# Performance work log

Hardware: AMD Instinct MI355X
Metric: run time of the kernel (lower is better)

## Reference

```python
import jax, jax.numpy as jnp
import numpy as np

N, L, S, C, H = 8, 1024, 1024, 256, 8
D = C // H  # 32

def setup_inputs() -> dict:
    key = jax.random.key(0)
    ks = jax.random.split(key, 9)
    sc = 1.0 / np.sqrt(C)
    return {
        "x": jax.random.normal(ks[0], (N, L, C), jnp.float32),
        "source1": jax.random.normal(ks[1], (N, S, C), jnp.float32),
        "x_embedding": jax.random.normal(ks[2], (N, L, C), jnp.float32),
        "source_embedding": jax.random.normal(ks[3], (N, S, C), jnp.float32),
        "Wq": jax.random.normal(ks[4], (C, C), jnp.float32) * sc,
        "Wk": jax.random.normal(ks[5], (C, C), jnp.float32) * sc,
        "Wv": jax.random.normal(ks[6], (C, C), jnp.float32) * sc,
        "Wp": jax.random.normal(ks[7], (C, C), jnp.float32) * sc,
        "bp": jnp.zeros((C,), jnp.float32),
    }

def reference(x, source1, x_embedding, source_embedding, Wq, Wk, Wv, Wp, bp):
    bs = x.shape[0]
    # torch `query += x_embedding` is IN-PLACE on x (same for source1),
    # so value projections also see embedding-added inputs.
    xq = x + x_embedding            # [N, L, C]
    sk = source1 + source_embedding  # [N, S, C]
    q = (xq @ Wq.T).reshape(bs, -1, H, D)   # [N, L, H, D]
    k = (sk @ Wk.T).reshape(bs, -1, H, D)   # [N, S, H, D]
    v1 = (xq @ Wv.T).reshape(bs, -1, H, D)  # [N, L, H, D]
    v2 = (sk @ Wv.T).reshape(bs, -1, H, D)  # [N, S, H, D]
    # Bilinear attention: softmax(q.k) aggregates v2, gated elementwise by v1.
    scores = jnp.einsum("nlhd,nshd->nlsh", q, k) / jnp.sqrt(jnp.float32(D))
    attn = jax.nn.softmax(scores, axis=2)          # softmax over source dim S
    message = v1 * jnp.einsum("nlsh,nshd->nlhd", attn, v2)  # [N, L, H, D]
    message = message.reshape(bs, -1, C)           # [N, L, C]
    return message @ Wp.T + bp
```

## Files before the change

kernel.cpp:

```cpp
#include <hip/hip_runtime.h>
#include <hip/hip_bf16.h>


typedef __bf16 bf16_t;
using bf16x8 = __attribute__((ext_vector_type(8))) __bf16;
using f32x4  = __attribute__((ext_vector_type(4))) float;

#define NB 8
#define LL 1024
#define SS 1024
#define CC 256
#define HH 8
#define DD 32
#define MTOK (NB * LL)

#define QSCALE (0.17677669529663688f * 1.4426950408889634f)

static __device__ __forceinline__ f32x4 mfma16(bf16x8 a, bf16x8 b, f32x4 c) {
  return __builtin_amdgcn_mfma_f32_16x16x32_bf16(a, b, c, 0, 0, 0);
}
static __device__ __forceinline__ float fexp2(float x) {
  return __builtin_amdgcn_exp2f(x);
}

__global__ __launch_bounds__(256) void wprep_kernel(
    const float* __restrict__ wq, const float* __restrict__ wk,
    const float* __restrict__ wv, const float* __restrict__ wp,
    bf16_t* __restrict__ Wall) {
  const int i = blockIdx.x * 256 + threadIdx.x;
  const int w = i >> 14, j = i & 16383;
  const float4* src = (const float4*)(w == 0 ? wq : w == 1 ? wk : w == 2 ? wv : wp);
  float4 v = src[j];
  bf16_t t4[4] __attribute__((aligned(8))) = {(bf16_t)v.x, (bf16_t)v.y,
                                              (bf16_t)v.z, (bf16_t)v.w};
  *(uint2*)(Wall + (size_t)w * CC * CC + 4 * (size_t)j) = *(const uint2*)t4;
}

__global__ __launch_bounds__(512) void proj_kernel(
    const float* __restrict__ x, const float* __restrict__ xe,
    const float* __restrict__ s1, const float* __restrict__ se,
    const bf16_t* __restrict__ Wall,
    bf16_t* __restrict__ Qw, bf16_t* __restrict__ Kw,
    bf16_t* __restrict__ V1w, bf16_t* __restrict__ V2T) {
  __shared__ __align__(16) bf16_t a_lds[64][264];

  const int tid = threadIdx.x;
  const int lane = tid & 63;
  const int wid = tid >> 6;
  const int r = lane & 15, g = lane >> 4;
  const int bm = blockIdx.x * 64;
  const int z = blockIdx.y;

  const float* A0 = z ? s1 : x;
  const float* A1 = z ? se : xe;
  const bf16_t* W0 = Wall + (size_t)z * CC * CC;
  const bf16_t* W1 = Wall + 2 * (size_t)CC * CC;

#pragma unroll
  for (int i = 0; i < 8; ++i) {
    const int f = i * 512 + tid;
    const int row = f >> 6, c4 = f & 63;
    float4 va = *(const float4*)(A0 + (size_t)(bm + row) * CC + c4 * 4);
    float4 vb = *(const float4*)(A1 + (size_t)(bm + row) * CC + c4 * 4);
    bf16_t t4[4] __attribute__((aligned(8))) = {
        (bf16_t)(va.x + vb.x), (bf16_t)(va.y + vb.y), (bf16_t)(va.z + vb.z),
        (bf16_t)(va.w + vb.w)};
    *(uint2*)&a_lds[row][c4 * 4] = *(const uint2*)t4;
  }
  __syncthreads();

  const int col_b0 = wid * 32;

  f32x4 acc0[4][2] = {};
  f32x4 acc1[4][2] = {};
#pragma unroll
  for (int k0 = 0; k0 < CC; k0 += 32) {
    bf16x8 a[4];
#pragma unroll
    for (int i = 0; i < 4; ++i)
      a[i] = *(const bf16x8*)&a_lds[i * 16 + r][k0 + g * 8];
    bf16x8 b00 = *(const bf16x8*)(W0 + (size_t)(col_b0 + r) * CC + k0 + g * 8);
    bf16x8 b01 = *(const bf16x8*)(W0 + (size_t)(col_b0 + 16 + r) * CC + k0 + g * 8);
    bf16x8 b10 = *(const bf16x8*)(W1 + (size_t)(col_b0 + r) * CC + k0 + g * 8);
    bf16x8 b11 = *(const bf16x8*)(W1 + (size_t)(col_b0 + 16 + r) * CC + k0 + g * 8);
#pragma unroll
    for (int i = 0; i < 4; ++i) {
      acc0[i][0] = mfma16(a[i], b00, acc0[i][0]);
      acc0[i][1] = mfma16(a[i], b01, acc0[i][1]);
      acc1[i][0] = mfma16(a[i], b10, acc1[i][0]);
      acc1[i][1] = mfma16(a[i], b11, acc1[i][1]);
    }
  }

#pragma unroll
  for (int i = 0; i < 4; ++i) {
#pragma unroll
    for (int j = 0; j < 2; ++j) {
      const int row_base = bm + i * 16 + g * 4;
      const int col = col_b0 + j * 16 + r;
      if (z == 0) {
#pragma unroll
        for (int t = 0; t < 4; ++t) {
          Qw[(size_t)(row_base + t) * CC + col] =
              (bf16_t)(acc0[i][j][t] * QSCALE);
          V1w[(size_t)(row_base + t) * CC + col] = (bf16_t)acc1[i][j][t];
        }
      } else {
#pragma unroll
        for (int t = 0; t < 4; ++t)
          Kw[(size_t)(row_base + t) * CC + col] = (bf16_t)acc0[i][j][t];
        const int n = row_base >> 10;
        const int s = row_base & (SS - 1);
        const int h = col >> 5;
        const int d = col & (DD - 1);
        bf16_t t4[4] __attribute__((aligned(8)));
#pragma unroll
        for (int t = 0; t < 4; ++t) t4[t] = (bf16_t)acc1[i][j][t];
        *(uint2*)(V2T + ((size_t)((n * HH + h) * DD + d)) * SS + s) =
            *(const uint2*)t4;
      }
    }
  }
}

__global__ __launch_bounds__(256) void attn_kernel(
    const bf16_t* __restrict__ Qw, const bf16_t* __restrict__ Kw,
    const bf16_t* __restrict__ V1w, const bf16_t* __restrict__ V2T,
    bf16_t* __restrict__ MSG) {
  __shared__ __align__(16) bf16_t k_lds[2][128][40];
  __shared__ __align__(16) bf16_t v_lds[2][32][136];
  __shared__ __align__(16) bf16_t p_sub[4][32][136];

  const int tid = threadIdx.x;
  const int lane = tid & 63;
  const int wid = tid >> 6;
  const int r = lane & 15, g = lane >> 4;

  const int bid = blockIdx.x;
  const int work = (bid & 7) * 64 + (bid >> 3);
  const int grp = work >> 3;
  const int lt = work & 7;
  const int n = grp >> 3;
  const int h = grp & 7;
  const int l0 = lt * 128;
  const size_t tokQ = (size_t)n * LL + l0 + wid * 32;

  const bf16x8 qf0 = *(const bf16x8*)(Qw + (tokQ + r) * CC + h * DD + g * 8);
  const bf16x8 qf1 = *(const bf16x8*)(Qw + (tokQ + 16 + r) * CC + h * DD + g * 8);
  const bf16_t* Kb = Kw + ((size_t)n * SS) * CC + h * DD;
  const bf16_t* Vt = V2T + ((size_t)(n * HH + h)) * DD * SS;

  const int ktr = tid >> 2, ktq = tid & 3;
  const int vtr = tid >> 3, vtq = tid & 7;

  float lr0 = 0.f, lr1 = 0.f;
  const f32x4 zero = {0.f, 0.f, 0.f, 0.f};
  f32x4 o00 = zero, o01 = zero;
  f32x4 o10 = zero, o11 = zero;

  uint4 kra = *(const uint4*)(Kb + (size_t)ktr * CC + ktq * 8);
  uint4 krb = *(const uint4*)(Kb + (size_t)(64 + ktr) * CC + ktq * 8);
  uint4 vra = *(const uint4*)(Vt + (size_t)vtr * SS + vtq * 8);
  uint4 vrb = *(const uint4*)(Vt + (size_t)vtr * SS + 64 + vtq * 8);
  *(uint4*)&k_lds[0][ktr][ktq * 8] = kra;
  *(uint4*)&k_lds[0][64 + ktr][ktq * 8] = krb;
  *(uint4*)&v_lds[0][vtr][vtq * 8] = vra;
  *(uint4*)&v_lds[0][vtr][64 + vtq * 8] = vrb;
  __syncthreads();

  for (int c = 0; c < 8; ++c) {
    const int cur = c & 1;
    if (c < 7) {
      const int s1 = (c + 1) * 128;
      kra = *(const uint4*)(Kb + (size_t)(s1 + ktr) * CC + ktq * 8);
      krb = *(const uint4*)(Kb + (size_t)(s1 + 64 + ktr) * CC + ktq * 8);
      vra = *(const uint4*)(Vt + (size_t)vtr * SS + s1 + vtq * 8);
      vrb = *(const uint4*)(Vt + (size_t)vtr * SS + s1 + 64 + vtq * 8);
    }

    f32x4 pt0[8], pt1[8];
#pragma unroll
    for (int m = 0; m < 8; ++m) {
      bf16x8 kf = *(const bf16x8*)&k_lds[cur][m * 16 + r][g * 8];
      pt0[m] = mfma16(kf, qf0, zero);
      pt1[m] = mfma16(kf, qf1, zero);
    }

#pragma unroll
    for (int m = 0; m < 8; ++m) {
      float a0 = fexp2(pt0[m][0]), a1 = fexp2(pt0[m][1]);
      float a2 = fexp2(pt0[m][2]), a3 = fexp2(pt0[m][3]);
      float b0 = fexp2(pt1[m][0]), b1 = fexp2(pt1[m][1]);
      float b2 = fexp2(pt1[m][2]), b3 = fexp2(pt1[m][3]);
      lr0 += (a0 + a1) + (a2 + a3);
      lr1 += (b0 + b1) + (b2 + b3);
      bf16_t pa[4] __attribute__((aligned(8))) = {(bf16_t)a0, (bf16_t)a1,
                                                  (bf16_t)a2, (bf16_t)a3};
      bf16_t pb[4] __attribute__((aligned(8))) = {(bf16_t)b0, (bf16_t)b1,
                                                  (bf16_t)b2, (bf16_t)b3};
      *(uint2*)&p_sub[wid][r][m * 16 + g * 4] = *(const uint2*)pa;
      *(uint2*)&p_sub[wid][16 + r][m * 16 + g * 4] = *(const uint2*)pb;
    }

#pragma unroll
    for (int u = 0; u < 4; ++u) {
      bf16x8 pf0 = *(const bf16x8*)&p_sub[wid][r][u * 32 + g * 8];
      bf16x8 pf1 = *(const bf16x8*)&p_sub[wid][16 + r][u * 32 + g * 8];
      bf16x8 va = *(const bf16x8*)&v_lds[cur][r][u * 32 + g * 8];
      bf16x8 vb = *(const bf16x8*)&v_lds[cur][16 + r][u * 32 + g * 8];
      o00 = mfma16(va, pf0, o00);
      o01 = mfma16(vb, pf0, o01);
      o10 = mfma16(va, pf1, o10);
      o11 = mfma16(vb, pf1, o11);
    }

    if (c < 7) {
      *(uint4*)&k_lds[cur ^ 1][ktr][ktq * 8] = kra;
      *(uint4*)&k_lds[cur ^ 1][64 + ktr][ktq * 8] = krb;
      *(uint4*)&v_lds[cur ^ 1][vtr][vtq * 8] = vra;
      *(uint4*)&v_lds[cur ^ 1][vtr][64 + vtq * 8] = vrb;
    }
    __syncthreads();
  }

  lr0 += __shfl_xor(lr0, 16);
  lr0 += __shfl_xor(lr0, 32);
  lr1 += __shfl_xor(lr1, 16);
  lr1 += __shfl_xor(lr1, 32);

  const float li0 = 1.f / lr0, li1 = 1.f / lr1;
  const bf16_t* V1b0 = V1w + (tokQ + r) * CC + h * DD;
  const bf16_t* V1b1 = V1w + (tokQ + 16 + r) * CC + h * DD;
  bf16_t* Mb0 = MSG + (tokQ + r) * CC + h * DD;
  bf16_t* Mb1 = MSG + (tokQ + 16 + r) * CC + h * DD;
  uint2 u00 = *(const uint2*)(V1b0 + g * 4);
  uint2 u01 = *(const uint2*)(V1b0 + 16 + g * 4);
  uint2 u10 = *(const uint2*)(V1b1 + g * 4);
  uint2 u11 = *(const uint2*)(V1b1 + 16 + g * 4);
  const bf16_t* v00 = (const bf16_t*)&u00;
  const bf16_t* v01 = (const bf16_t*)&u01;
  const bf16_t* v10 = (const bf16_t*)&u10;
  const bf16_t* v11 = (const bf16_t*)&u11;
  bf16_t w00[4] __attribute__((aligned(8))), w01[4] __attribute__((aligned(8)));
  bf16_t w10[4] __attribute__((aligned(8))), w11[4] __attribute__((aligned(8)));
#pragma unroll
  for (int i = 0; i < 4; ++i) {
    w00[i] = (bf16_t)(o00[i] * li0 * (float)v00[i]);
    w01[i] = (bf16_t)(o01[i] * li0 * (float)v01[i]);
    w10[i] = (bf16_t)(o10[i] * li1 * (float)v10[i]);
    w11[i] = (bf16_t)(o11[i] * li1 * (float)v11[i]);
  }
  *(uint2*)(Mb0 + g * 4) = *(const uint2*)w00;
  *(uint2*)(Mb0 + 16 + g * 4) = *(const uint2*)w01;
  *(uint2*)(Mb1 + g * 4) = *(const uint2*)w10;
  *(uint2*)(Mb1 + 16 + g * 4) = *(const uint2*)w11;
}

__global__ __launch_bounds__(512) void out_kernel(
    const bf16_t* __restrict__ MSG, const bf16_t* __restrict__ Wp,
    const float* __restrict__ bp, float* __restrict__ out) {
  __shared__ __align__(16) bf16_t a_lds[64][264];

  const int tid = threadIdx.x;
  const int lane = tid & 63;
  const int wid = tid >> 6;
  const int r = lane & 15, g = lane >> 4;
  const int bm = blockIdx.x * 64;

#pragma unroll
  for (int i = 0; i < 4; ++i) {
    const int f = i * 512 + tid;
    const int row = f >> 5, c8 = f & 31;
    uint4 v = *(const uint4*)(MSG + (size_t)(bm + row) * CC + c8 * 8);
    *(uint4*)&a_lds[row][c8 * 8] = v;
  }
  __syncthreads();

  const int col_b0 = wid * 32;

  f32x4 acc[4][2] = {};
#pragma unroll
  for (int k0 = 0; k0 < CC; k0 += 32) {
    bf16x8 a[4];
#pragma unroll
    for (int i = 0; i < 4; ++i)
      a[i] = *(const bf16x8*)&a_lds[i * 16 + r][k0 + g * 8];
    bf16x8 b0 = *(const bf16x8*)(Wp + (size_t)(col_b0 + r) * CC + k0 + g * 8);
    bf16x8 b1 = *(const bf16x8*)(Wp + (size_t)(col_b0 + 16 + r) * CC + k0 + g * 8);
#pragma unroll
    for (int i = 0; i < 4; ++i) {
      acc[i][0] = mfma16(a[i], b0, acc[i][0]);
      acc[i][1] = mfma16(a[i], b1, acc[i][1]);
    }
  }

#pragma unroll
  for (int i = 0; i < 4; ++i) {
#pragma unroll
    for (int j = 0; j < 2; ++j) {
      const int row_base = bm + i * 16 + g * 4;
      const int col = col_b0 + j * 16 + r;
      const float bv = bp[col];
#pragma unroll
      for (int t = 0; t < 4; ++t)
        out[(size_t)(row_base + t) * CC + col] = acc[i][j][t] + bv;
    }
  }
}

extern "C" void kernel_launch(void* const* d_in, const int* in_sizes, int n_in,
                              void* d_out, int out_size, void* d_ws,
                              size_t ws_size, hipStream_t stream) {
  const float* x  = (const float*)d_in[0];
  const float* s1 = (const float*)d_in[1];
  const float* xe = (const float*)d_in[2];
  const float* se = (const float*)d_in[3];
  const float* Wq = (const float*)d_in[4];
  const float* Wk = (const float*)d_in[5];
  const float* Wv = (const float*)d_in[6];
  const float* Wp = (const float*)d_in[7];
  const float* bp = (const float*)d_in[8];
  float* out = (float*)d_out;

  char* ws = (char*)d_ws;
  bf16_t* Wall = (bf16_t*)(ws);
  bf16_t* Qw   = (bf16_t*)(ws + (1u << 20));
  bf16_t* Kw   = (bf16_t*)(ws + (5u << 20));
  bf16_t* V1w  = (bf16_t*)(ws + (9u << 20));
  bf16_t* V2T  = (bf16_t*)(ws + (13u << 20));
  bf16_t* MSG  = (bf16_t*)(ws + (17u << 20));
  bf16_t* Wpb  = Wall + 3 * CC * CC;

  wprep_kernel<<<256, 256, 0, stream>>>(Wq, Wk, Wv, Wp, Wall);
  proj_kernel<<<dim3(MTOK / 64, 2), 512, 0, stream>>>(
      x, xe, s1, se, Wall, Qw, Kw, V1w, V2T);
  attn_kernel<<<512, 256, 0, stream>>>(Qw, Kw, V1w, V2T, MSG);
  out_kernel<<<MTOK / 64, 512, 0, stream>>>(MSG, Wpb, bp, out);
}
```

Baseline: 54.78 us.

## Keep softmax probabilities in registers via permuted K layout, use 8 waves

```diff
diff --git a/kernel.cpp b/kernel.cpp
--- a/kernel.cpp
+++ b/kernel.cpp
@@ -123,13 +123,12 @@
   }
 }
 
-__global__ __launch_bounds__(256) void attn_kernel(
+__global__ __launch_bounds__(512) void attn_kernel(
     const bf16_t* __restrict__ Qw, const bf16_t* __restrict__ Kw,
     const bf16_t* __restrict__ V1w, const bf16_t* __restrict__ V2T,
     bf16_t* __restrict__ MSG) {
   __shared__ __align__(16) bf16_t k_lds[2][128][40];
   __shared__ __align__(16) bf16_t v_lds[2][32][136];
-  __shared__ __align__(16) bf16_t p_sub[4][32][136];
 
   const int tid = threadIdx.x;
   const int lane = tid & 63;
@@ -143,29 +142,24 @@
   const int n = grp >> 3;
   const int h = grp & 7;
   const int l0 = lt * 128;
-  const size_t tokQ = (size_t)n * LL + l0 + wid * 32;
-
-  const bf16x8 qf0 = *(const bf16x8*)(Qw + (tokQ + r) * CC + h * DD + g * 8);
-  const bf16x8 qf1 = *(const bf16x8*)(Qw + (tokQ + 16 + r) * CC + h * DD + g * 8);
+  const size_t tokQ = (size_t)n * LL + l0 + wid * 16;
+
+  const bf16x8 qf = *(const bf16x8*)(Qw + (tokQ + r) * CC + h * DD + g * 8);
   const bf16_t* Kb = Kw + ((size_t)n * SS) * CC + h * DD;
   const bf16_t* Vt = V2T + ((size_t)(n * HH + h)) * DD * SS;
 
   const int ktr = tid >> 2, ktq = tid & 3;
-  const int vtr = tid >> 3, vtq = tid & 7;
-
-  float lr0 = 0.f, lr1 = 0.f;
+  const int kpr = (ktr & 96) | ((ktr & 4) << 2) | ((ktr & 24) >> 1) | (ktr & 3);
+  const int vtr = tid >> 4, vtq = tid & 15;
+
+  float lr = 0.f;
   const f32x4 zero = {0.f, 0.f, 0.f, 0.f};
-  f32x4 o00 = zero, o01 = zero;
-  f32x4 o10 = zero, o11 = zero;
+  f32x4 o0 = zero, o1 = zero;
 
   uint4 kra = *(const uint4*)(Kb + (size_t)ktr * CC + ktq * 8);
-  uint4 krb = *(const uint4*)(Kb + (size_t)(64 + ktr) * CC + ktq * 8);
   uint4 vra = *(const uint4*)(Vt + (size_t)vtr * SS + vtq * 8);
-  uint4 vrb = *(const uint4*)(Vt + (size_t)vtr * SS + 64 + vtq * 8);
-  *(uint4*)&k_lds[0][ktr][ktq * 8] = kra;
-  *(uint4*)&k_lds[0][64 + ktr][ktq * 8] = krb;
+  *(uint4*)&k_lds[0][kpr][ktq * 8] = kra;
   *(uint4*)&v_lds[0][vtr][vtq * 8] = vra;
-  *(uint4*)&v_lds[0][vtr][64 + vtq * 8] = vrb;
   __syncthreads();
 
   for (int c = 0; c < 8; ++c) {
@@ -173,87 +167,58 @@
     if (c < 7) {
       const int s1 = (c + 1) * 128;
       kra = *(const uint4*)(Kb + (size_t)(s1 + ktr) * CC + ktq * 8);
-      krb = *(const uint4*)(Kb + (size_t)(s1 + 64 + ktr) * CC + ktq * 8);
       vra = *(const uint4*)(Vt + (size_t)vtr * SS + s1 + vtq * 8);
-      vrb = *(const uint4*)(Vt + (size_t)vtr * SS + s1 + 64 + vtq * 8);
-    }
-
-    f32x4 pt0[8], pt1[8];
+    }
+
+    f32x4 pt[8];
 #pragma unroll
     for (int m = 0; m < 8; ++m) {
       bf16x8 kf = *(const bf16x8*)&k_lds[cur][m * 16 + r][g * 8];
-      pt0[m] = mfma16(kf, qf0, zero);
-      pt1[m] = mfma16(kf, qf1, zero);
-    }
-
-#pragma unroll
-    for (int m = 0; m < 8; ++m) {
-      float a0 = fexp2(pt0[m][0]), a1 = fexp2(pt0[m][1]);
-      float a2 = fexp2(pt0[m][2]), a3 = fexp2(pt0[m][3]);
-      float b0 = fexp2(pt1[m][0]), b1 = fexp2(pt1[m][1]);
-      float b2 = fexp2(pt1[m][2]), b3 = fexp2(pt1[m][3]);
-      lr0 += (a0 + a1) + (a2 + a3);
-      lr1 += (b0 + b1) + (b2 + b3);
-      bf16_t pa[4] __attribute__((aligned(8))) = {(bf16_t)a0, (bf16_t)a1,
-                                                  (bf16_t)a2, (bf16_t)a3};
-      bf16_t pb[4] __attribute__((aligned(8))) = {(bf16_t)b0, (bf16_t)b1,
-                                                  (bf16_t)b2, (bf16_t)b3};
-      *(uint2*)&p_sub[wid][r][m * 16 + g * 4] = *(const uint2*)pa;
-      *(uint2*)&p_sub[wid][16 + r][m * 16 + g * 4] = *(const uint2*)pb;
-    }
-
-#pragma unroll
-    for (int u = 0; u < 4; ++u) {
-      bf16x8 pf0 = *(const bf16x8*)&p_sub[wid][r][u * 32 + g * 8];
-      bf16x8 pf1 = *(const bf16x8*)&p_sub[wid][16 + r][u * 32 + g * 8];
-      bf16x8 va = *(const bf16x8*)&v_lds[cur][r][u * 32 + g * 8];
-      bf16x8 vb = *(const bf16x8*)&v_lds[cur][16 + r][u * 32 + g * 8];
-      o00 = mfma16(va, pf0, o00);
-      o01 = mfma16(vb, pf0, o01);
-      o10 = mfma16(va, pf1, o10);
-      o11 = mfma16(vb, pf1, o11);
+      pt[m] = mfma16(kf, qf, zero);
+    }
+
+#pragma unroll
+    for (int t = 0; t < 4; ++t) {
+      float p0 = fexp2(pt[2 * t][0]), p1 = fexp2(pt[2 * t][1]);
+      float p2 = fexp2(pt[2 * t][2]), p3 = fexp2(pt[2 * t][3]);
+      float p4 = fexp2(pt[2 * t + 1][0]), p5 = fexp2(pt[2 * t + 1][1]);
+      float p6 = fexp2(pt[2 * t + 1][2]), p7 = fexp2(pt[2 * t + 1][3]);
+      lr += ((p0 + p1) + (p2 + p3)) + ((p4 + p5) + (p6 + p7));
+      bf16_t pb[8] __attribute__((aligned(16))) = {
+          (bf16_t)p0, (bf16_t)p1, (bf16_t)p2, (bf16_t)p3,
+          (bf16_t)p4, (bf16_t)p5, (bf16_t)p6, (bf16_t)p7};
+      bf16x8 pf = *(const bf16x8*)pb;
+      bf16x8 va = *(const bf16x8*)&v_lds[cur][r][t * 32 + g * 8];
+      bf16x8 vb = *(const bf16x8*)&v_lds[cur][16 + r][t * 32 + g * 8];
+      o0 = mfma16(va, pf, o0);
+      o1 = mfma16(vb, pf, o1);
     }
 
     if (c < 7) {
-      *(uint4*)&k_lds[cur ^ 1][ktr][ktq * 8] = kra;
-      *(uint4*)&k_lds[cur ^ 1][64 + ktr][ktq * 8] = krb;
+      *(uint4*)&k_lds[cur ^ 1][kpr][ktq * 8] = kra;
       *(uint4*)&v_lds[cur ^ 1][vtr][vtq * 8] = vra;
-      *(uint4*)&v_lds[cur ^ 1][vtr][64 + vtq * 8] = vrb;
     }
     __syncthreads();
   }
 
-  lr0 += __shfl_xor(lr0, 16);
-  lr0 += __shfl_xor(lr0, 32);
-  lr1 += __shfl_xor(lr1, 16);
-  lr1 += __shfl_xor(lr1, 32);
-
-  const float li0 = 1.f / lr0, li1 = 1.f / lr1;
-  const bf16_t* V1b0 = V1w + (tokQ + r) * CC + h * DD;
-  const bf16_t* V1b1 = V1w + (tokQ + 16 + r) * CC + h * DD;
-  bf16_t* Mb0 = MSG + (tokQ + r) * CC + h * DD;
-  bf16_t* Mb1 = MSG + (tokQ + 16 + r) * CC + h * DD;
-  uint2 u00 = *(const uint2*)(V1b0 + g * 4);
-  uint2 u01 = *(const uint2*)(V1b0 + 16 + g * 4);
-  uint2 u10 = *(const uint2*)(V1b1 + g * 4);
-  uint2 u11 = *(const uint2*)(V1b1 + 16 + g * 4);
-  const bf16_t* v00 = (const bf16_t*)&u00;
-  const bf16_t* v01 = (const bf16_t*)&u01;
-  const bf16_t* v10 = (const bf16_t*)&u10;
-  const bf16_t* v11 = (const bf16_t*)&u11;
-  bf16_t w00[4] __attribute__((aligned(8))), w01[4] __attribute__((aligned(8)));
-  bf16_t w10[4] __attribute__((aligned(8))), w11[4] __attribute__((aligned(8)));
+  lr += __shfl_xor(lr, 16);
+  lr += __shfl_xor(lr, 32);
+  const float li = 1.f / lr;
+
+  const bf16_t* V1b = V1w + (tokQ + r) * CC + h * DD;
+  bf16_t* Mb = MSG + (tokQ + r) * CC + h * DD;
+  uint2 u0 = *(const uint2*)(V1b + g * 4);
+  uint2 u1 = *(const uint2*)(V1b + 16 + g * 4);
+  const bf16_t* v0 = (const bf16_t*)&u0;
+  const bf16_t* v1 = (const bf16_t*)&u1;
+  bf16_t w0[4] __attribute__((aligned(8))), w1[4] __attribute__((aligned(8)));
 #pragma unroll
   for (int i = 0; i < 4; ++i) {
-    w00[i] = (bf16_t)(o00[i] * li0 * (float)v00[i]);
-    w01[i] = (bf16_t)(o01[i] * li0 * (float)v01[i]);
-    w10[i] = (bf16_t)(o10[i] * li1 * (float)v10[i]);
-    w11[i] = (bf16_t)(o11[i] * li1 * (float)v11[i]);
-  }
-  *(uint2*)(Mb0 + g * 4) = *(const uint2*)w00;
-  *(uint2*)(Mb0 + 16 + g * 4) = *(const uint2*)w01;
-  *(uint2*)(Mb1 + g * 4) = *(const uint2*)w10;
-  *(uint2*)(Mb1 + 16 + g * 4) = *(const uint2*)w11;
+    w0[i] = (bf16_t)(o0[i] * li * (float)v0[i]);
+    w1[i] = (bf16_t)(o1[i] * li * (float)v1[i]);
+  }
+  *(uint2*)(Mb + g * 4) = *(const uint2*)w0;
+  *(uint2*)(Mb + 16 + g * 4) = *(const uint2*)w1;
 }
 
 __global__ __launch_bounds__(512) void out_kernel(
@@ -334,6 +299,6 @@
   wprep_kernel<<<256, 256, 0, stream>>>(Wq, Wk, Wv, Wp, Wall);
   proj_kernel<<<dim3(MTOK / 64, 2), 512, 0, stream>>>(
       x, xe, s1, se, Wall, Qw, Kw, V1w, V2T);
-  attn_kernel<<<512, 256, 0, stream>>>(Qw, Kw, V1w, V2T, MSG);
+  attn_kernel<<<512, 512, 0, stream>>>(Qw, Kw, V1w, V2T, MSG);
   out_kernel<<<MTOK / 64, 512, 0, stream>>>(MSG, Wpb, bp, out);
 }
```

Result: faster. 52.15 us (-4.8%).

## Keep softmax probabilities in registers via permuted K rows and larger blocks

Applied to the files above, without the earlier changes.

```diff
diff --git a/kernel.cpp b/kernel.cpp
--- a/kernel.cpp
+++ b/kernel.cpp
@@ -123,13 +123,12 @@
   }
 }
 
-__global__ __launch_bounds__(256) void attn_kernel(
+__global__ __launch_bounds__(512) void attn_kernel(
     const bf16_t* __restrict__ Qw, const bf16_t* __restrict__ Kw,
     const bf16_t* __restrict__ V1w, const bf16_t* __restrict__ V2T,
     bf16_t* __restrict__ MSG) {
   __shared__ __align__(16) bf16_t k_lds[2][128][40];
   __shared__ __align__(16) bf16_t v_lds[2][32][136];
-  __shared__ __align__(16) bf16_t p_sub[4][32][136];
 
   const int tid = threadIdx.x;
   const int lane = tid & 63;
@@ -137,21 +136,23 @@
   const int r = lane & 15, g = lane >> 4;
 
   const int bid = blockIdx.x;
-  const int work = (bid & 7) * 64 + (bid >> 3);
-  const int grp = work >> 3;
-  const int lt = work & 7;
+  const int work = (bid & 7) * 32 + (bid >> 3);
+  const int grp = work >> 2;
+  const int lt = work & 3;
   const int n = grp >> 3;
   const int h = grp & 7;
-  const int l0 = lt * 128;
+  const int l0 = lt * 256;
   const size_t tokQ = (size_t)n * LL + l0 + wid * 32;
 
   const bf16x8 qf0 = *(const bf16x8*)(Qw + (tokQ + r) * CC + h * DD + g * 8);
-  const bf16x8 qf1 = *(const bf16x8*)(Qw + (tokQ + 16 + r) * CC + h * DD + g * 8);
+  const bf16x8 qf1 =
+      *(const bf16x8*)(Qw + (tokQ + 16 + r) * CC + h * DD + g * 8);
   const bf16_t* Kb = Kw + ((size_t)n * SS) * CC + h * DD;
   const bf16_t* Vt = V2T + ((size_t)(n * HH + h)) * DD * SS;
 
   const int ktr = tid >> 2, ktq = tid & 3;
-  const int vtr = tid >> 3, vtq = tid & 7;
+  const int kpr = (ktr & 96) | ((ktr & 4) << 2) | ((ktr & 24) >> 1) | (ktr & 3);
+  const int vtr = tid >> 4, vtq = tid & 15;
 
   float lr0 = 0.f, lr1 = 0.f;
   const f32x4 zero = {0.f, 0.f, 0.f, 0.f};
@@ -159,13 +160,9 @@
   f32x4 o10 = zero, o11 = zero;
 
   uint4 kra = *(const uint4*)(Kb + (size_t)ktr * CC + ktq * 8);
-  uint4 krb = *(const uint4*)(Kb + (size_t)(64 + ktr) * CC + ktq * 8);
   uint4 vra = *(const uint4*)(Vt + (size_t)vtr * SS + vtq * 8);
-  uint4 vrb = *(const uint4*)(Vt + (size_t)vtr * SS + 64 + vtq * 8);
-  *(uint4*)&k_lds[0][ktr][ktq * 8] = kra;
-  *(uint4*)&k_lds[0][64 + ktr][ktq * 8] = krb;
+  *(uint4*)&k_lds[0][kpr][ktq * 8] = kra;
   *(uint4*)&v_lds[0][vtr][vtq * 8] = vra;
-  *(uint4*)&v_lds[0][vtr][64 + vtq * 8] = vrb;
   __syncthreads();
 
   for (int c = 0; c < 8; ++c) {
@@ -173,9 +170,7 @@
     if (c < 7) {
       const int s1 = (c + 1) * 128;
       kra = *(const uint4*)(Kb + (size_t)(s1 + ktr) * CC + ktq * 8);
-      krb = *(const uint4*)(Kb + (size_t)(s1 + 64 + ktr) * CC + ktq * 8);
       vra = *(const uint4*)(Vt + (size_t)vtr * SS + s1 + vtq * 8);
-      vrb = *(const uint4*)(Vt + (size_t)vtr * SS + s1 + 64 + vtq * 8);
     }
 
     f32x4 pt0[8], pt1[8];
@@ -187,27 +182,27 @@
     }
 
 #pragma unroll
-    for (int m = 0; m < 8; ++m) {
-      float a0 = fexp2(pt0[m][0]), a1 = fexp2(pt0[m][1]);
-      float a2 = fexp2(pt0[m][2]), a3 = fexp2(pt0[m][3]);
-      float b0 = fexp2(pt1[m][0]), b1 = fexp2(pt1[m][1]);
-      float b2 = fexp2(pt1[m][2]), b3 = fexp2(pt1[m][3]);
-      lr0 += (a0 + a1) + (a2 + a3);
-      lr1 += (b0 + b1) + (b2 + b3);
-      bf16_t pa[4] __attribute__((aligned(8))) = {(bf16_t)a0, (bf16_t)a1,
-                                                  (bf16_t)a2, (bf16_t)a3};
-      bf16_t pb[4] __attribute__((aligned(8))) = {(bf16_t)b0, (bf16_t)b1,
-                                                  (bf16_t)b2, (bf16_t)b3};
-      *(uint2*)&p_sub[wid][r][m * 16 + g * 4] = *(const uint2*)pa;
-      *(uint2*)&p_sub[wid][16 + r][m * 16 + g * 4] = *(const uint2*)pb;
-    }
-
-#pragma unroll
-    for (int u = 0; u < 4; ++u) {
-      bf16x8 pf0 = *(const bf16x8*)&p_sub[wid][r][u * 32 + g * 8];
-      bf16x8 pf1 = *(const bf16x8*)&p_sub[wid][16 + r][u * 32 + g * 8];
-      bf16x8 va = *(const bf16x8*)&v_lds[cur][r][u * 32 + g * 8];
-      bf16x8 vb = *(const bf16x8*)&v_lds[cur][16 + r][u * 32 + g * 8];
+    for (int t = 0; t < 4; ++t) {
+      float a0 = fexp2(pt0[2 * t][0]), a1 = fexp2(pt0[2 * t][1]);
+      float a2 = fexp2(pt0[2 * t][2]), a3 = fexp2(pt0[2 * t][3]);
+      float a4 = fexp2(pt0[2 * t + 1][0]), a5 = fexp2(pt0[2 * t + 1][1]);
+      float a6 = fexp2(pt0[2 * t + 1][2]), a7 = fexp2(pt0[2 * t + 1][3]);
+      float b0 = fexp2(pt1[2 * t][0]), b1 = fexp2(pt1[2 * t][1]);
+      float b2 = fexp2(pt1[2 * t][2]), b3 = fexp2(pt1[2 * t][3]);
+      float b4 = fexp2(pt1[2 * t + 1][0]), b5 = fexp2(pt1[2 * t + 1][1]);
+      float b6 = fexp2(pt1[2 * t + 1][2]), b7 = fexp2(pt1[2 * t + 1][3]);
+      lr0 += ((a0 + a1) + (a2 + a3)) + ((a4 + a5) + (a6 + a7));
+      lr1 += ((b0 + b1) + (b2 + b3)) + ((b4 + b5) + (b6 + b7));
+      bf16_t pa[8] __attribute__((aligned(16))) = {
+          (bf16_t)a0, (bf16_t)a1, (bf16_t)a2, (bf16_t)a3,
+          (bf16_t)a4, (bf16_t)a5, (bf16_t)a6, (bf16_t)a7};
+      bf16_t pb[8] __attribute__((aligned(16))) = {
+          (bf16_t)b0, (bf16_t)b1, (bf16_t)b2, (bf16_t)b3,
+          (bf16_t)b4, (bf16_t)b5, (bf16_t)b6, (bf16_t)b7};
+      bf16x8 pf0 = *(const bf16x8*)pa;
+      bf16x8 pf1 = *(const bf16x8*)pb;
+      bf16x8 va = *(const bf16x8*)&v_lds[cur][r][t * 32 + g * 8];
+      bf16x8 vb = *(const bf16x8*)&v_lds[cur][16 + r][t * 32 + g * 8];
       o00 = mfma16(va, pf0, o00);
       o01 = mfma16(vb, pf0, o01);
       o10 = mfma16(va, pf1, o10);
@@ -215,10 +210,8 @@
     }
 
     if (c < 7) {
-      *(uint4*)&k_lds[cur ^ 1][ktr][ktq * 8] = kra;
-      *(uint4*)&k_lds[cur ^ 1][64 + ktr][ktq * 8] = krb;
+      *(uint4*)&k_lds[cur ^ 1][kpr][ktq * 8] = kra;
       *(uint4*)&v_lds[cur ^ 1][vtr][vtq * 8] = vra;
-      *(uint4*)&v_lds[cur ^ 1][vtr][64 + vtq * 8] = vrb;
     }
     __syncthreads();
   }
@@ -227,8 +220,8 @@
   lr0 += __shfl_xor(lr0, 32);
   lr1 += __shfl_xor(lr1, 16);
   lr1 += __shfl_xor(lr1, 32);
-
   const float li0 = 1.f / lr0, li1 = 1.f / lr1;
+
   const bf16_t* V1b0 = V1w + (tokQ + r) * CC + h * DD;
   const bf16_t* V1b1 = V1w + (tokQ + 16 + r) * CC + h * DD;
   bf16_t* Mb0 = MSG + (tokQ + r) * CC + h * DD;
@@ -334,6 +327,6 @@
   wprep_kernel<<<256, 256, 0, stream>>>(Wq, Wk, Wv, Wp, Wall);
   proj_kernel<<<dim3(MTOK / 64, 2), 512, 0, stream>>>(
       x, xe, s1, se, Wall, Qw, Kw, V1w, V2T);
-  attn_kernel<<<512, 256, 0, stream>>>(Qw, Kw, V1w, V2T, MSG);
+  attn_kernel<<<256, 512, 0, stream>>>(Qw, Kw, V1w, V2T, MSG);
   out_kernel<<<MTOK / 64, 512, 0, stream>>>(MSG, Wpb, bp, out);
 }
```

Result: faster. 49.50 us (-9.6%).
